# Kernel optimization log

Measured on AMD Instinct MI355X. Metric: run time of the kernel, lower is better.

The kernel has to match this reference:

```python
import jax, jax.numpy as jnp
import numpy as np

N_NODES = 50000
N_EDGES = 800000
D = 64
H = 128


def setup_inputs() -> dict:
    key = jax.random.key(0)
    ks = jax.random.split(key, 6)
    x = jax.random.normal(ks[0], (N_NODES, D), dtype=jnp.float32)
    edge_index = jax.random.randint(ks[1], (2, N_EDGES), 0, N_NODES, dtype=jnp.int64)
    # GIN MLP params (Linear(D->H) -> ReLU -> Linear(H->D))
    W1 = jax.random.normal(ks[2], (D, H), dtype=jnp.float32) * (1.0 / np.sqrt(D))
    b1 = jnp.zeros((H,), dtype=jnp.float32)
    W2 = jax.random.normal(ks[3], (H, D), dtype=jnp.float32) * (1.0 / np.sqrt(H))
    b2 = jnp.zeros((D,), dtype=jnp.float32)
    eps = jnp.zeros((1, 1), dtype=jnp.float32)  # trainable eps parameter
    return {"x": x, "W1": W1, "b1": b1, "W2": W2, "b2": b2, "eps": eps,
            "edge_index": edge_index}


def reference(x, W1, b1, W2, b2, eps, edge_index):
    src, dst = edge_index[0], edge_index[1]
    # node -> edge gather (0th-order ptensor on each edge = sum of endpoint feats)
    msg = x[src] + x[dst]                                    # [E, D]
    # edge -> node gather: each node sums messages of its incident edges
    agg = (jax.ops.segment_sum(msg, src, num_segments=N_NODES)
           + jax.ops.segment_sum(msg, dst, num_segments=N_NODES))  # [N, D]
    ones = jnp.ones((N_EDGES,), dtype=x.dtype)
    deg = (jax.ops.segment_sum(ones, src, num_segments=N_NODES)
           + jax.ops.segment_sum(ones, dst, num_segments=N_NODES))  # [N]
    # subtract deg*x so aggregation reduces to the plain neighbor sum (GIN)
    neighbor = agg - x * deg[:, None]
    out = (1.0 + eps) * x + neighbor                          # eps is [1,1], broadcasts
    # GIN MLP
    h = jax.nn.relu(out @ W1 + b1)
    return h @ W2 + b2
```

## Files before the change

### kernel.cpp

```cpp
#include <hip/hip_runtime.h>


#define D 64
#define H 128
#define MPW 8
#define REGSH 6
#define REGSZ 64
#define P1_BLOCKS 256
#define EVBUF_SZ 6400
#define NR_MAX 1024
#define NCAP 96
#define PSTR 68

typedef __attribute__((ext_vector_type(8))) short short8;
typedef __attribute__((ext_vector_type(4))) float float4v;

__device__ __forceinline__ float lane_bcast(float v, int l) {
    return __uint_as_float(__builtin_amdgcn_readlane(__float_as_uint(v), l));
}

__device__ __forceinline__ unsigned short f2bf(float f) {
    unsigned int u = __float_as_uint(f);
    u = (u + (((u >> 16) & 1u) + 0x7fffu)) >> 16;
    return (unsigned short)u;
}

__device__ __forceinline__ void bf2_acc(unsigned int u, float& a, float& b) {
    a += __uint_as_float(u << 16);
    b += __uint_as_float(u & 0xffff0000u);
}

__global__ void zero_int_kernel(int* __restrict__ p, int n) {
    int i = blockIdx.x * blockDim.x + threadIdx.x;
    if (i < n) p[i] = 0;
}

__global__ void zero_f_kernel(float* __restrict__ p, int n) {
    int i = blockIdx.x * blockDim.x + threadIdx.x;
    if (i < n) p[i] = 0.0f;
}

__global__ void prep_kernel(unsigned int* __restrict__ xh2, int npairs,
                            int* __restrict__ cursor, int NR, int CAPB,
                            const float* __restrict__ W1,
                            const float* __restrict__ W2,
                            unsigned short* __restrict__ wsW1,
                            unsigned short* __restrict__ wsW2) {
    int i = blockIdx.x * blockDim.x + threadIdx.x;
    if (i < NR) cursor[i] = i * CAPB;
    if (i < 32) xh2[npairs + i] = 0;
    if (i < 8192) {
        int j = i & 7, ln = (i >> 3) & 63;
        int q = (ln >> 4) & 3;
        int tt1 = (i >> 9) & 7, s1 = i >> 12;
        wsW1[i] = f2bf(W1[(s1 * 32 + q * 8 + j) * H + tt1 * 16 + (ln & 15)]);
        int tt2 = (i >> 9) & 3, s2 = i >> 11;
        wsW2[i] = f2bf(W2[(s2 * 32 + q * 8 + j) * D + tt2 * 16 + (ln & 15)]);
    }
}

__global__ __launch_bounds__(256) void part1_kernel(
    const int* __restrict__ src, const int* __restrict__ dst,
    int* __restrict__ cursor, unsigned int* __restrict__ evarr,
    const float* __restrict__ x, unsigned int* __restrict__ xh2, int npairs,
    int E, int N, int NR, int CAPB, int EPB)
{
    __shared__ unsigned int evbuf[EVBUF_SZ];
    __shared__ unsigned int sortbuf[EVBUF_SZ];
    __shared__ unsigned short tickbuf[EVBUF_SZ];
    __shared__ int hist[NR_MAX];
    __shared__ int lbase[NR_MAX];
    __shared__ int gbase[NR_MAX];
    __shared__ int scanw[256];
    int t = threadIdx.x;

    int gstride = gridDim.x * 256;
    for (int i = blockIdx.x * 256 + t; i < npairs; i += gstride) {
        float2 v = *(const float2*)(x + (size_t)i * 2);
        unsigned int a = __float_as_uint(v.x);
        unsigned int b = __float_as_uint(v.y);
        a = (a + (((a >> 16) & 1u) + 0x7fffu)) >> 16;
        b = (b + (((b >> 16) & 1u) + 0x7fffu)) >> 16;
        xh2[i] = a | (b << 16);
    }

    for (int b = t; b < NR; b += 256) hist[b] = 0;
    __syncthreads();

    int e0 = blockIdx.x * EPB;
    int ne = E - e0; if (ne > EPB) ne = EPB; if (ne < 0) ne = 0;
    for (int i = t; i < ne; i += 256) {
        int s = src[e0 + i], d = dst[e0 + i];
        s = (s < 0) ? 0 : ((s >= N) ? N - 1 : s);
        d = (d < 0) ? 0 : ((d >= N) ? N - 1 : d);
        unsigned int ev0 = ((unsigned int)s << 16) | (unsigned int)d;
        unsigned int ev1 = ((unsigned int)d << 16) | (unsigned int)s;
        int k0 = atomicAdd(&hist[s >> REGSH], 1);
        int k1 = atomicAdd(&hist[d >> REGSH], 1);
        evbuf[2 * i]     = ev0; tickbuf[2 * i]     = (unsigned short)k0;
        evbuf[2 * i + 1] = ev1; tickbuf[2 * i + 1] = (unsigned short)k1;
    }
    __syncthreads();

    {
        int i0 = t * 4;
        int h0 = (i0 + 0 < NR) ? hist[i0 + 0] : 0;
        int h1 = (i0 + 1 < NR) ? hist[i0 + 1] : 0;
        int h2 = (i0 + 2 < NR) ? hist[i0 + 2] : 0;
        int h3 = (i0 + 3 < NR) ? hist[i0 + 3] : 0;
        int s4 = h0 + h1 + h2 + h3;
        scanw[t] = s4;
        __syncthreads();
        for (int off = 1; off < 256; off <<= 1) {
            int u = (t >= off) ? scanw[t - off] : 0;
            __syncthreads();
            scanw[t] += u;
            __syncthreads();
        }
        int run = scanw[t] - s4;
        if (i0 + 0 < NR) { lbase[i0 + 0] = run; run += h0; }
        if (i0 + 1 < NR) { lbase[i0 + 1] = run; run += h1; }
        if (i0 + 2 < NR) { lbase[i0 + 2] = run; run += h2; }
        if (i0 + 3 < NR) { lbase[i0 + 3] = run; run += h3; }
    }

    for (int b = t; b < NR; b += 256) {
        int c = hist[b];
        gbase[b] = c ? atomicAdd(&cursor[b], c) : 0;
    }
    __syncthreads();

    int nev = 2 * ne;
    for (int i = t; i < nev; i += 256) {
        unsigned int ev = evbuf[i];
        int reg = (int)(ev >> (16 + REGSH));
        sortbuf[lbase[reg] + (int)tickbuf[i]] = ev;
    }
    __syncthreads();

    for (int i = t; i < nev; i += 256) {
        unsigned int ev = sortbuf[i];
        int reg = (int)(ev >> (16 + REGSH));
        int addr = gbase[reg] + (i - lbase[reg]);
        if (addr < (reg + 1) * CAPB) evarr[addr] = ev;
    }
}

__global__ __launch_bounds__(512, 8) void part2_fused(
    const unsigned int* __restrict__ evarr, const int* __restrict__ cursor,
    const unsigned short* __restrict__ xh, const float* __restrict__ x,
    const float* __restrict__ epsp,
    const unsigned short* __restrict__ wsW1,
    const unsigned short* __restrict__ wsW2,
    const float* __restrict__ b1, const float* __restrict__ b2,
    float* __restrict__ y, int N, int CAPB)
{
    __shared__ unsigned short nbuf[REGSZ * NCAP + 32];
    __shared__ int scnt[REGSZ];
    __shared__ float pre_lds[REGSZ * PSTR];
    int t = threadIdx.x;
    int b = blockIdx.x;
    if (t < REGSZ) scnt[t] = 0;
    __syncthreads();

    int base = b * CAPB;
    int count = cursor[b] - base;
    if (count < 0) count = 0;
    if (count > CAPB) count = CAPB;

    for (int i = t; i < count; i += 512) {
        unsigned int ev = evarr[base + i];
        int row = (int)((ev >> 16) & (REGSZ - 1));
        int k = atomicAdd(&scnt[row], 1);
        if (k < NCAP) nbuf[row * NCAP + k] = (unsigned short)(ev & 0xffffu);
    }
    __syncthreads();

    int wave = t >> 6, lane = t & 63;
    int r = lane >> 5;
    int h = lane & 31;
    float e1 = 1.0f + epsp[0];

    for (int k = 0; k < 8; ++k) {
        int n = wave * 8 + k;
        int v = b * REGSZ + n;
        int m = (v < N) ? scnt[n] : 0;
        m = (m > NCAP) ? NCAP : m;
        float f0 = 0.0f, f1 = 0.0f;
        for (int j = 0; j < m; j += 32) {
            int cc[16];
#pragma unroll
            for (int q = 0; q < 16; ++q) {
                int ii = j + 2 * q + r;
                int c = (int)nbuf[n * NCAP + ii];
                cc[q] = (ii < m) ? c : N;
            }
            unsigned int u[16];
#pragma unroll
            for (int q = 0; q < 16; ++q)
                u[q] = *(const unsigned int*)(xh + (size_t)cc[q] * D + 2 * h);
#pragma unroll
            for (int q = 0; q < 16; ++q) bf2_acc(u[q], f0, f1);
        }
        f0 += __shfl_xor(f0, 32, 64);
        f1 += __shfl_xor(f1, 32, 64);
        if (r == 0) {
            float2 sv = make_float2(0.0f, 0.0f);
            if (v < N) sv = *(const float2*)(x + (size_t)v * D + 2 * h);
            pre_lds[n * PSTR + 2 * h]     = f0 + e1 * sv.x;
            pre_lds[n * PSTR + 2 * h + 1] = f1 + e1 * sv.y;
        }
    }
    __syncthreads();

    int p = wave >> 1, hh = wave & 1;
    int quad = lane >> 4, lm = lane & 15;
    int row0 = p * 16 + lm;

    short8 a1f[2];
#pragma unroll
    for (int s = 0; s < 2; ++s) {
        const float* rp = &pre_lds[row0 * PSTR + s * 32 + quad * 8];
        float4v p0 = *(const float4v*)rp;
        float4v p1 = *(const float4v*)(rp + 4);
        short8 a;
        a[0] = (short)f2bf(p0[0]); a[1] = (short)f2bf(p0[1]);
        a[2] = (short)f2bf(p0[2]); a[3] = (short)f2bf(p0[3]);
        a[4] = (short)f2bf(p1[0]); a[5] = (short)f2bf(p1[1]);
        a[6] = (short)f2bf(p1[2]); a[7] = (short)f2bf(p1[3]);
        a1f[s] = a;
    }
    __syncthreads();

    unsigned short* hbuf = (unsigned short*)pre_lds;

    float4v acc1[4];
#pragma unroll
    for (int i = 0; i < 4; ++i) {
        int tt = hh * 4 + i;
        float bb = b1[tt * 16 + lm];
        float4v c = {bb, bb, bb, bb};
#pragma unroll
        for (int s = 0; s < 2; ++s) {
            short8 bw = *(const short8*)&wsW1[((s * 8 + tt) * 64 + lane) * 8];
            c = __builtin_amdgcn_mfma_f32_16x16x32_bf16(a1f[s], bw, c, 0, 0, 0);
        }
        acc1[i] = c;
    }

    unsigned short* hb = &hbuf[p * 16 * H];
#pragma unroll
    for (int i = 0; i < 4; ++i) {
        int tt = hh * 4 + i;
#pragma unroll
        for (int rr = 0; rr < 4; ++rr) {
            float hv = fmaxf(acc1[i][rr], 0.0f);
            hb[(quad * 4 + rr) * H + tt * 16 + lm] = f2bf(hv);
        }
    }
    __syncthreads();

    short8 a2[4];
#pragma unroll
    for (int s = 0; s < 4; ++s)
        a2[s] = *(const short8*)&hb[lm * H + s * 32 + quad * 8];

    int v0t = b * REGSZ + p * 16;
#pragma unroll
    for (int i = 0; i < 2; ++i) {
        int tt = hh * 2 + i;
        float bb = b2[tt * 16 + lm];
        float4v c = {bb, bb, bb, bb};
#pragma unroll
        for (int s = 0; s < 4; ++s) {
            short8 bw = *(const short8*)&wsW2[((s * 4 + tt) * 64 + lane) * 8];
            c = __builtin_amdgcn_mfma_f32_16x16x32_bf16(a2[s], bw, c, 0, 0, 0);
        }
#pragma unroll
        for (int rr = 0; rr < 4; ++rr) {
            int v = v0t + quad * 4 + rr;
            if (v < N) y[(size_t)v * D + tt * 16 + lm] = c[rr];
        }
    }
}


__global__ void count_kernel(const int* __restrict__ ei, int* __restrict__ deg,
                             int twoE, int N) {
    int i = blockIdx.x * blockDim.x + threadIdx.x;
    if (i < twoE) {
        int v = ei[i];
        v = (v < 0) ? 0 : ((v >= N) ? N - 1 : v);
        atomicAdd(&deg[v], 1);
    }
}

__global__ __launch_bounds__(256) void scan_part1(const int* __restrict__ deg,
                                                  int* __restrict__ bsum, int n) {
    __shared__ int red[256];
    int t = threadIdx.x;
    int i = blockIdx.x * 256 + t;
    red[t] = (i < n) ? deg[i] : 0;
    __syncthreads();
    for (int off = 128; off > 0; off >>= 1) {
        if (t < off) red[t] += red[t + off];
        __syncthreads();
    }
    if (t == 0) bsum[blockIdx.x] = red[0];
}

__global__ __launch_bounds__(256) void scan_part2(const int* __restrict__ bsum,
                                                  int* __restrict__ boff,
                                                  int* __restrict__ rowstart_n, int nb) {
    __shared__ int s[256];
    int t = threadIdx.x;
    int v = (t < nb) ? bsum[t] : 0;
    s[t] = v;
    __syncthreads();
    for (int off = 1; off < 256; off <<= 1) {
        int u = (t >= off) ? s[t - off] : 0;
        __syncthreads();
        s[t] += u;
        __syncthreads();
    }
    if (t < nb) boff[t] = s[t] - v;
    if (t == 255) *rowstart_n = s[255];
}

__global__ __launch_bounds__(256) void scan_part3(const int* __restrict__ deg,
                                                  const int* __restrict__ boff,
                                                  int* __restrict__ rowstart,
                                                  int* __restrict__ cursor, int n) {
    __shared__ int s[256];
    int t = threadIdx.x;
    int i = blockIdx.x * 256 + t;
    int v = (i < n) ? deg[i] : 0;
    s[t] = v;
    __syncthreads();
    for (int off = 1; off < 256; off <<= 1) {
        int u = (t >= off) ? s[t - off] : 0;
        __syncthreads();
        s[t] += u;
        __syncthreads();
    }
    if (i < n) {
        int r = boff[blockIdx.x] + s[t] - v;
        rowstart[i] = r;
        cursor[i] = r;
    }
}

__global__ __launch_bounds__(256) void scan_single(const int* __restrict__ deg,
                                                   int* __restrict__ rowstart,
                                                   int* __restrict__ cursor,
                                                   int n, int chunk) {
    __shared__ int psum[256];
    int t = threadIdx.x;
    int lo = t * chunk;
    int hi = lo + chunk; if (hi > n) hi = n;
    int s = 0;
    for (int i = lo; i < hi; ++i) s += deg[i];
    psum[t] = s;
    __syncthreads();
    for (int off = 1; off < 256; off <<= 1) {
        int v = (t >= off) ? psum[t - off] : 0;
        __syncthreads();
        psum[t] += v;
        __syncthreads();
    }
    int run = (t == 0) ? 0 : psum[t - 1];
    for (int i = lo; i < hi; ++i) {
        int d = deg[i];
        rowstart[i] = run;
        cursor[i] = run;
        run += d;
    }
    if (t == 255) rowstart[n] = psum[255];
}

__global__ __launch_bounds__(256) void fill_xcd(
    const int* __restrict__ src, const int* __restrict__ dst,
    int* __restrict__ cursor, int* __restrict__ col,
    int E, int N, int npg)
{
    int grp = blockIdx.x & 7;
    int slice = blockIdx.x >> 3;
    int lo = grp * npg;
    int hi = lo + npg; if (hi > N) hi = N;
    int stride = (gridDim.x >> 3) * 256;
    for (int i = slice * 256 + threadIdx.x; i < E; i += stride) {
        int s = src[i], d = dst[i];
        s = (s < 0) ? 0 : ((s >= N) ? N - 1 : s);
        d = (d < 0) ? 0 : ((d >= N) ? N - 1 : d);
        if (s >= lo && s < hi) { int p = atomicAdd(&cursor[s], 1); col[p] = d; }
        if (d >= lo && d < hi) { int q = atomicAdd(&cursor[d], 1); col[q] = s; }
    }
}

__global__ __launch_bounds__(256) void gather_csr2(
    const float* __restrict__ x, const float* __restrict__ epsp,
    const int* __restrict__ rowstart, const int* __restrict__ col,
    float* __restrict__ pre, int N)
{
    int wid = (blockIdx.x * 256 + threadIdx.x) >> 6;
    int lane = threadIdx.x & 63;
    int v0 = wid * 2;
    if (v0 >= N) return;
    int v1 = v0 + 1;
    float eps1 = 1.0f + epsp[0];
    int j0 = rowstart[v0], re0 = rowstart[v0 + 1];
    float a0 = eps1 * x[(size_t)v0 * D + lane];
    int j1 = 0, re1 = 0;
    float a1 = 0.0f;
    if (v1 < N) {
        j1 = rowstart[v1]; re1 = rowstart[v1 + 1];
        a1 = eps1 * x[(size_t)v1 * D + lane];
    }
    while (j0 + 8 <= re0 && j1 + 8 <= re1) {
        float p0 = x[(size_t)col[j0 + 0] * D + lane];
        float p1 = x[(size_t)col[j0 + 1] * D + lane];
        float p2 = x[(size_t)col[j0 + 2] * D + lane];
        float p3 = x[(size_t)col[j0 + 3] * D + lane];
        float p4 = x[(size_t)col[j0 + 4] * D + lane];
        float p5 = x[(size_t)col[j0 + 5] * D + lane];
        float p6 = x[(size_t)col[j0 + 6] * D + lane];
        float p7 = x[(size_t)col[j0 + 7] * D + lane];
        float q0 = x[(size_t)col[j1 + 0] * D + lane];
        float q1 = x[(size_t)col[j1 + 1] * D + lane];
        float q2 = x[(size_t)col[j1 + 2] * D + lane];
        float q3 = x[(size_t)col[j1 + 3] * D + lane];
        float q4 = x[(size_t)col[j1 + 4] * D + lane];
        float q5 = x[(size_t)col[j1 + 5] * D + lane];
        float q6 = x[(size_t)col[j1 + 6] * D + lane];
        float q7 = x[(size_t)col[j1 + 7] * D + lane];
        a0 += ((p0 + p1) + (p2 + p3)) + ((p4 + p5) + (p6 + p7));
        a1 += ((q0 + q1) + (q2 + q3)) + ((q4 + q5) + (q6 + q7));
        j0 += 8; j1 += 8;
    }
    for (; j0 + 8 <= re0; j0 += 8) {
        float p0 = x[(size_t)col[j0 + 0] * D + lane];
        float p1 = x[(size_t)col[j0 + 1] * D + lane];
        float p2 = x[(size_t)col[j0 + 2] * D + lane];
        float p3 = x[(size_t)col[j0 + 3] * D + lane];
        float p4 = x[(size_t)col[j0 + 4] * D + lane];
        float p5 = x[(size_t)col[j0 + 5] * D + lane];
        float p6 = x[(size_t)col[j0 + 6] * D + lane];
        float p7 = x[(size_t)col[j0 + 7] * D + lane];
        a0 += ((p0 + p1) + (p2 + p3)) + ((p4 + p5) + (p6 + p7));
    }
    for (; j1 + 8 <= re1; j1 += 8) {
        float q0 = x[(size_t)col[j1 + 0] * D + lane];
        float q1 = x[(size_t)col[j1 + 1] * D + lane];
        float q2 = x[(size_t)col[j1 + 2] * D + lane];
        float q3 = x[(size_t)col[j1 + 3] * D + lane];
        float q4 = x[(size_t)col[j1 + 4] * D + lane];
        float q5 = x[(size_t)col[j1 + 5] * D + lane];
        float q6 = x[(size_t)col[j1 + 6] * D + lane];
        float q7 = x[(size_t)col[j1 + 7] * D + lane];
        a1 += ((q0 + q1) + (q2 + q3)) + ((q4 + q5) + (q6 + q7));
    }
    for (; j0 < re0; ++j0) a0 += x[(size_t)col[j0] * D + lane];
    for (; j1 < re1; ++j1) a1 += x[(size_t)col[j1] * D + lane];
    pre[(size_t)v0 * D + lane] = a0;
    if (v1 < N) pre[(size_t)v1 * D + lane] = a1;
}

__device__ __forceinline__ void mlp_store(
    const float* acc, float* sW, int v0, int t, int lane, int nNodes,
    const float* __restrict__ W2,
    const float* __restrict__ b1, const float* __restrict__ b2,
    float* __restrict__ y)
{
    float b1a = b1[lane], b1b = b1[lane + 64];
    float ha[MPW], hb[MPW];
#pragma unroll
    for (int m = 0; m < MPW; ++m) { ha[m] = b1a; hb[m] = b1b; }
#pragma unroll 4
    for (int f = 0; f < D; ++f) {
        float wa = sW[f * H + lane];
        float wb = sW[f * H + lane + 64];
#pragma unroll
        for (int m = 0; m < MPW; ++m) {
            float o = lane_bcast(acc[m], f);
            ha[m] += o * wa;
            hb[m] += o * wb;
        }
    }
#pragma unroll
    for (int m = 0; m < MPW; ++m) {
        ha[m] = fmaxf(ha[m], 0.0f);
        hb[m] = fmaxf(hb[m], 0.0f);
    }

    __syncthreads();
    for (int i = t; i < H * D; i += 256) sW[i] = W2[i];
    __syncthreads();

    float b2v = b2[lane];
    float yv[MPW];
#pragma unroll
    for (int m = 0; m < MPW; ++m) yv[m] = b2v;
#pragma unroll 4
    for (int k = 0; k < 64; ++k) {
        float w = sW[k * D + lane];
#pragma unroll
        for (int m = 0; m < MPW; ++m) yv[m] += lane_bcast(ha[m], k) * w;
    }
#pragma unroll 4
    for (int k = 0; k < 64; ++k) {
        float w = sW[(k + 64) * D + lane];
#pragma unroll
        for (int m = 0; m < MPW; ++m) yv[m] += lane_bcast(hb[m], k) * w;
    }
#pragma unroll
    for (int m = 0; m < MPW; ++m) {
        int v = v0 + m;
        if (v < nNodes) y[(size_t)v * D + lane] = yv[m];
    }
}

__global__ __launch_bounds__(256) void mlp_pre(
    const float* __restrict__ pre, const float* __restrict__ W1,
    const float* __restrict__ b1, const float* __restrict__ W2,
    const float* __restrict__ b2, float* __restrict__ y, int nNodes)
{
    __shared__ float sW[D * H];
    int t = threadIdx.x;
    for (int i = t; i < D * H; i += 256) sW[i] = W1[i];
    __syncthreads();
    int wave = t >> 6, lane = t & 63;
    int v0 = (blockIdx.x * 4 + wave) * MPW;
    float acc[MPW];
#pragma unroll
    for (int m = 0; m < MPW; ++m) {
        int v = v0 + m;
        acc[m] = (v < nNodes) ? pre[(size_t)v * D + lane] : 0.0f;
    }
    mlp_store(acc, sW, v0, t, lane, nNodes, W2, b1, b2, y);
}

__global__ __launch_bounds__(256) void gather_mlp_csr(
    const float* __restrict__ x, const float* __restrict__ W1,
    const float* __restrict__ b1, const float* __restrict__ W2,
    const float* __restrict__ b2, const float* __restrict__ epsp,
    const int* __restrict__ rowstart, const int* __restrict__ col,
    float* __restrict__ y, int nNodes)
{
    __shared__ float sW[D * H];
    int t = threadIdx.x;
    for (int i = t; i < D * H; i += 256) sW[i] = W1[i];
    __syncthreads();
    int wave = t >> 6, lane = t & 63;
    float eps1 = 1.0f + epsp[0];
    int v0 = (blockIdx.x * 4 + wave) * MPW;
    float acc[MPW];
#pragma unroll
    for (int m = 0; m < MPW; ++m) {
        int v = v0 + m;
        float a = 0.0f;
        if (v < nNodes) {
            int rs = rowstart[v], re = rowstart[v + 1];
            a = eps1 * x[(size_t)v * D + lane];
            int j = rs;
            for (; j + 8 <= re; j += 8) {
                float p0 = x[(size_t)col[j + 0] * D + lane];
                float p1 = x[(size_t)col[j + 1] * D + lane];
                float p2 = x[(size_t)col[j + 2] * D + lane];
                float p3 = x[(size_t)col[j + 3] * D + lane];
                float p4 = x[(size_t)col[j + 4] * D + lane];
                float p5 = x[(size_t)col[j + 5] * D + lane];
                float p6 = x[(size_t)col[j + 6] * D + lane];
                float p7 = x[(size_t)col[j + 7] * D + lane];
                a += ((p0 + p1) + (p2 + p3)) + ((p4 + p5) + (p6 + p7));
            }
            for (; j < re; ++j) a += x[(size_t)col[j] * D + lane];
        }
        acc[m] = a;
    }
    mlp_store(acc, sW, v0, t, lane, nNodes, W2, b1, b2, y);
}

__global__ void scatter_kernel(const float* __restrict__ x,
                               const int* __restrict__ src,
                               const int* __restrict__ dst,
                               float* __restrict__ agg, int E, int N)
{
    int tid = blockIdx.x * blockDim.x + threadIdx.x;
    int e = tid >> 6, lane = tid & 63;
    if (e < E) {
        int s = src[e], d = dst[e];
        s = (s < 0) ? 0 : ((s >= N) ? N - 1 : s);
        d = (d < 0) ? 0 : ((d >= N) ? N - 1 : d);
        float xs = x[(size_t)s * D + lane];
        float xd = x[(size_t)d * D + lane];
        atomicAdd(&agg[(size_t)s * D + lane], xd);
        atomicAdd(&agg[(size_t)d * D + lane], xs);
    }
}

__global__ __launch_bounds__(256) void mlp_from_agg(
    const float* __restrict__ x, const float* __restrict__ W1,
    const float* __restrict__ b1, const float* __restrict__ W2,
    const float* __restrict__ b2, const float* __restrict__ epsp,
    float* __restrict__ yio, int nNodes)
{
    __shared__ float sW[D * H];
    int t = threadIdx.x;
    for (int i = t; i < D * H; i += 256) sW[i] = W1[i];
    __syncthreads();
    int wave = t >> 6, lane = t & 63;
    float eps1 = 1.0f + epsp[0];
    int v0 = (blockIdx.x * 4 + wave) * MPW;
    float acc[MPW];
#pragma unroll
    for (int m = 0; m < MPW; ++m) {
        int v = v0 + m;
        acc[m] = (v < nNodes)
                   ? (eps1 * x[(size_t)v * D + lane] + yio[(size_t)v * D + lane])
                   : 0.0f;
    }
    mlp_store(acc, sW, v0, t, lane, nNodes, W2, b1, b2, yio);
}

extern "C" void kernel_launch(void* const* d_in, const int* in_sizes, int n_in,
                              void* d_out, int out_size, void* d_ws, size_t ws_size,
                              hipStream_t stream)
{
    const float* x   = (const float*)d_in[0];
    const float* W1  = (const float*)d_in[1];
    const float* b1  = (const float*)d_in[2];
    const float* W2  = (const float*)d_in[3];
    const float* b2  = (const float*)d_in[4];
    const float* eps = (const float*)d_in[5];
    const int*   ei  = (const int*)d_in[6];
    float* out = (float*)d_out;

    int N = in_sizes[0] / D;
    int E = in_sizes[6] / 2;
    const int* src = ei;
    const int* dst = ei + E;

    int nb = (N + 255) / 256;

    int NR = (N + REGSZ - 1) >> REGSH;
    int meanE = (NR > 0) ? (2 * E + NR - 1) / NR : 0;
    int CAPB = meanE + meanE / 4 + 128;
    int EPB = (E + P1_BLOCKS - 1) / P1_BLOCKS;
    size_t off_cur  = 0;
    size_t off_ev   = (off_cur + (size_t)NR * 4 + 15) & ~(size_t)15;
    size_t off_xh   = (off_ev + (size_t)NR * CAPB * 4 + 15) & ~(size_t)15;
    size_t off_w1   = (off_xh + (size_t)(N + 1) * D * 2 + 15) & ~(size_t)15;
    size_t off_w2   = off_w1 + 8192 * 2;
    size_t need_part = off_w2 + 8192 * 2;

    size_t csr_ints = (size_t)(3 * N + 1 + 2 * E) + 512;
    size_t need_csr = csr_ints * sizeof(int);
    size_t need_split = need_csr + (size_t)N * D * sizeof(float);
    int mlp_blocks = (N + 4 * MPW - 1) / (4 * MPW);

    if (ws_size >= need_part && N >= REGSZ && N <= 65535
        && NR <= NR_MAX && 2 * EPB <= EVBUF_SZ && (N * D) % 2 == 0) {
        char* base = (char*)d_ws;
        int*            cursor = (int*)(base + off_cur);
        unsigned int*   evarr  = (unsigned int*)(base + off_ev);
        unsigned short* xh     = (unsigned short*)(base + off_xh);
        unsigned short* wsW1   = (unsigned short*)(base + off_w1);
        unsigned short* wsW2   = (unsigned short*)(base + off_w2);
        int npairs = N * D / 2;

        prep_kernel<<<32, 256, 0, stream>>>(
            (unsigned int*)xh, npairs, cursor, NR, CAPB, W1, W2, wsW1, wsW2);
        part1_kernel<<<P1_BLOCKS, 256, 0, stream>>>(
            src, dst, cursor, evarr, x, (unsigned int*)xh, npairs,
            E, N, NR, CAPB, EPB);
        part2_fused<<<NR, 512, 0, stream>>>(
            evarr, cursor, xh, x, eps, wsW1, wsW2, b1, b2, out, N, CAPB);
    } else if (ws_size >= need_csr) {
        int*   deg      = (int*)d_ws;
        int*   cursor   = deg + N;
        int*   rowstart = cursor + N;
        int*   col      = rowstart + (N + 1);
        int*   bsum     = col + 2 * E;
        int*   boff     = bsum + 256;
        float* pre      = (float*)(boff + 256);

        zero_int_kernel<<<(N + 255) / 256, 256, 0, stream>>>(deg, N);
        count_kernel<<<(2 * E + 255) / 256, 256, 0, stream>>>(ei, deg, 2 * E, N);
        if (nb <= 256) {
            scan_part1<<<nb, 256, 0, stream>>>(deg, bsum, N);
            scan_part2<<<1, 256, 0, stream>>>(bsum, boff, &rowstart[N], nb);
            scan_part3<<<nb, 256, 0, stream>>>(deg, boff, rowstart, cursor, N);
        } else {
            int chunk = (N + 255) / 256;
            scan_single<<<1, 256, 0, stream>>>(deg, rowstart, cursor, N, chunk);
        }
        fill_xcd<<<2048, 256, 0, stream>>>(src, dst, cursor, col, E, N, (N + 7) / 8);
        int waves = (N + 1) / 2;
        int gather_blocks = (waves + 3) / 4;
        if (ws_size >= need_split) {
            gather_csr2<<<gather_blocks, 256, 0, stream>>>(x, eps, rowstart, col, pre, N);
            mlp_pre<<<mlp_blocks, 256, 0, stream>>>(pre, W1, b1, W2, b2, out, N);
        } else {
            gather_mlp_csr<<<mlp_blocks, 256, 0, stream>>>(
                x, W1, b1, W2, b2, eps, rowstart, col, out, N);
        }
    } else {
        int nd = N * D;
        zero_f_kernel<<<(nd + 255) / 256, 256, 0, stream>>>(out, nd);
        long long st = (long long)E * 64;
        scatter_kernel<<<(int)((st + 255) / 256), 256, 0, stream>>>(x, src, dst, out, E, N);
        mlp_from_agg<<<mlp_blocks, 256, 0, stream>>>(x, W1, b1, W2, b2, eps, out, N);
    }
}
```

Baseline: 141.5 us.

## Move bf16 conversion of x into prep kernel and widen part1 blocks to 1024 threads

The fp32-to-bf16 packing of x moves out of part1_kernel into prep_kernel, which now launches 1024 blocks instead of 32, so the conversion is spread over many more threads. part1_kernel now runs 1024 threads per block, so each block's edge bucketing, its histogram scan (now one bin per thread) and its scatter loops are spread over four times as many threads. The intent is to cut part1's serial per-block work and its occupancy limit from large shared buffers. In exchange the scan needs more barrier steps, and the conversion now runs serially before part1 instead of inside it.

```diff
diff --git a/kernel.cpp b/kernel.cpp
--- a/kernel.cpp
+++ b/kernel.cpp
@@ -7,6 +7,7 @@
 #define REGSH 6
 #define REGSZ 64
 #define P1_BLOCKS 256
+#define P1_THREADS 1024
 #define EVBUF_SZ 6400
 #define NR_MAX 1024
 #define NCAP 96
@@ -40,13 +41,23 @@
     if (i < n) p[i] = 0.0f;
 }
 
-__global__ void prep_kernel(unsigned int* __restrict__ xh2, int npairs,
+__global__ void prep_kernel(const float* __restrict__ x,
+                            unsigned int* __restrict__ xh2, int npairs,
                             int* __restrict__ cursor, int NR, int CAPB,
                             const float* __restrict__ W1,
                             const float* __restrict__ W2,
                             unsigned short* __restrict__ wsW1,
                             unsigned short* __restrict__ wsW2) {
     int i = blockIdx.x * blockDim.x + threadIdx.x;
+    int gs = gridDim.x * blockDim.x;
+    for (int k = i; k < npairs; k += gs) {
+        float2 v = *(const float2*)(x + (size_t)k * 2);
+        unsigned int a = __float_as_uint(v.x);
+        unsigned int b = __float_as_uint(v.y);
+        a = (a + (((a >> 16) & 1u) + 0x7fffu)) >> 16;
+        b = (b + (((b >> 16) & 1u) + 0x7fffu)) >> 16;
+        xh2[k] = a | (b << 16);
+    }
     if (i < NR) cursor[i] = i * CAPB;
     if (i < 32) xh2[npairs + i] = 0;
     if (i < 8192) {
@@ -59,10 +70,9 @@
     }
 }
 
-__global__ __launch_bounds__(256) void part1_kernel(
+__global__ __launch_bounds__(P1_THREADS) void part1_kernel(
     const int* __restrict__ src, const int* __restrict__ dst,
     int* __restrict__ cursor, unsigned int* __restrict__ evarr,
-    const float* __restrict__ x, unsigned int* __restrict__ xh2, int npairs,
     int E, int N, int NR, int CAPB, int EPB)
 {
     __shared__ unsigned int evbuf[EVBUF_SZ];
@@ -71,25 +81,15 @@
     __shared__ int hist[NR_MAX];
     __shared__ int lbase[NR_MAX];
     __shared__ int gbase[NR_MAX];
-    __shared__ int scanw[256];
-    int t = threadIdx.x;
-
-    int gstride = gridDim.x * 256;
-    for (int i = blockIdx.x * 256 + t; i < npairs; i += gstride) {
-        float2 v = *(const float2*)(x + (size_t)i * 2);
-        unsigned int a = __float_as_uint(v.x);
-        unsigned int b = __float_as_uint(v.y);
-        a = (a + (((a >> 16) & 1u) + 0x7fffu)) >> 16;
-        b = (b + (((b >> 16) & 1u) + 0x7fffu)) >> 16;
-        xh2[i] = a | (b << 16);
-    }
-
-    for (int b = t; b < NR; b += 256) hist[b] = 0;
+    __shared__ int scanw[P1_THREADS];
+    int t = threadIdx.x;
+
+    for (int b = t; b < NR; b += P1_THREADS) hist[b] = 0;
     __syncthreads();
 
     int e0 = blockIdx.x * EPB;
     int ne = E - e0; if (ne > EPB) ne = EPB; if (ne < 0) ne = 0;
-    for (int i = t; i < ne; i += 256) {
+    for (int i = t; i < ne; i += P1_THREADS) {
         int s = src[e0 + i], d = dst[e0 + i];
         s = (s < 0) ? 0 : ((s >= N) ? N - 1 : s);
         d = (d < 0) ? 0 : ((d >= N) ? N - 1 : d);
@@ -103,42 +103,33 @@
     __syncthreads();
 
     {
-        int i0 = t * 4;
-        int h0 = (i0 + 0 < NR) ? hist[i0 + 0] : 0;
-        int h1 = (i0 + 1 < NR) ? hist[i0 + 1] : 0;
-        int h2 = (i0 + 2 < NR) ? hist[i0 + 2] : 0;
-        int h3 = (i0 + 3 < NR) ? hist[i0 + 3] : 0;
-        int s4 = h0 + h1 + h2 + h3;
-        scanw[t] = s4;
+        int h0 = (t < NR) ? hist[t] : 0;
+        scanw[t] = h0;
         __syncthreads();
-        for (int off = 1; off < 256; off <<= 1) {
+        for (int off = 1; off < P1_THREADS; off <<= 1) {
             int u = (t >= off) ? scanw[t - off] : 0;
             __syncthreads();
             scanw[t] += u;
             __syncthreads();
         }
-        int run = scanw[t] - s4;
-        if (i0 + 0 < NR) { lbase[i0 + 0] = run; run += h0; }
-        if (i0 + 1 < NR) { lbase[i0 + 1] = run; run += h1; }
-        if (i0 + 2 < NR) { lbase[i0 + 2] = run; run += h2; }
-        if (i0 + 3 < NR) { lbase[i0 + 3] = run; run += h3; }
-    }
-
-    for (int b = t; b < NR; b += 256) {
+        if (t < NR) lbase[t] = scanw[t] - h0;
+    }
+
+    for (int b = t; b < NR; b += P1_THREADS) {
         int c = hist[b];
         gbase[b] = c ? atomicAdd(&cursor[b], c) : 0;
     }
     __syncthreads();
 
     int nev = 2 * ne;
-    for (int i = t; i < nev; i += 256) {
+    for (int i = t; i < nev; i += P1_THREADS) {
         unsigned int ev = evbuf[i];
         int reg = (int)(ev >> (16 + REGSH));
         sortbuf[lbase[reg] + (int)tickbuf[i]] = ev;
     }
     __syncthreads();
 
-    for (int i = t; i < nev; i += 256) {
+    for (int i = t; i < nev; i += P1_THREADS) {
         unsigned int ev = sortbuf[i];
         int reg = (int)(ev >> (16 + REGSH));
         int addr = gbase[reg] + (i - lbase[reg]);
@@ -668,11 +659,10 @@
         unsigned short* wsW2   = (unsigned short*)(base + off_w2);
         int npairs = N * D / 2;
 
-        prep_kernel<<<32, 256, 0, stream>>>(
-            (unsigned int*)xh, npairs, cursor, NR, CAPB, W1, W2, wsW1, wsW2);
-        part1_kernel<<<P1_BLOCKS, 256, 0, stream>>>(
-            src, dst, cursor, evarr, x, (unsigned int*)xh, npairs,
-            E, N, NR, CAPB, EPB);
+        prep_kernel<<<1024, 256, 0, stream>>>(
+            x, (unsigned int*)xh, npairs, cursor, NR, CAPB, W1, W2, wsW1, wsW2);
+        part1_kernel<<<P1_BLOCKS, P1_THREADS, 0, stream>>>(
+            src, dst, cursor, evarr, E, N, NR, CAPB, EPB);
         part2_fused<<<NR, 512, 0, stream>>>(
             evarr, cursor, xh, x, eps, wsW1, wsW2, b1, b2, out, N, CAPB);
     } else if (ws_size >= need_csr) {
```

New measurement: 134.6 us. 1.05x faster.
